# Kernel tuning notes

Hardware: AMD Instinct MI355X
Metric: run time of the kernel (lower is better)

## Reference

```python
import math
import jax, jax.numpy as jnp
import numpy as np

B, M, N = 32, 64, 5000   # batch, multi_width (POMO rollouts), n_nodes
L, H, D, E = 100, 8, 16, 128  # local_size, head_num, qkv_dim, emb_dim


def setup_inputs() -> dict:
    key = jax.random.key(0)
    ks = jax.random.split(key, 10)
    return {
        "dist": jax.random.uniform(ks[0], (B, M, N), jnp.float32),
        "theta": jax.random.uniform(ks[1], (B, M, N), jnp.float32, minval=-math.pi, maxval=math.pi),
        "ninf_mask": jnp.zeros((B, M, N), jnp.float32),
        "W_init": jax.random.normal(ks[2], (E, 2), jnp.float32) * 0.1,
        "b_init": jax.random.normal(ks[3], (E,), jnp.float32) * 0.1,
        "cur_token": jax.random.uniform(ks[4], (E,), jnp.float32, minval=-1.0, maxval=1.0),
        "Wq": jax.random.normal(ks[5], (H * D, E), jnp.float32) * 0.05,
        "Wk": jax.random.normal(ks[6], (H * D, E), jnp.float32) * 0.05,
        "Wv": jax.random.normal(ks[7], (H * D, E), jnp.float32) * 0.05,
        "Wc": jax.random.normal(ks[8], (E, H * D), jnp.float32) * 0.05,
        "bc": jax.random.normal(ks[9], (E,), jnp.float32) * 0.05,
    }


def _positional_signal():
    # transformer sinusoidal encoding over the L gathered neighbors (E even -> no pad)
    num_ts = E // 2
    log_inc = math.log(10000.0) / max(num_ts - 1, 1)
    inv_ts = jnp.exp(jnp.arange(num_ts, dtype=jnp.float32) * -log_inc)
    pos = jnp.arange(L, dtype=jnp.float32)
    scaled = pos[:, None] * inv_ts[None, :]            # [L, E/2]
    return jnp.concatenate([jnp.sin(scaled), jnp.cos(scaled)], axis=1)  # [L, E]


def reference(dist, theta, ninf_mask, W_init, b_init, cur_token, Wq, Wk, Wv, Wc, bc):
    # mask out infeasible nodes (dist - (-inf) = +inf pushes them out of top-k)
    d = dist - ninf_mask                               # [B, M, N]
    neg_vals, idx = jax.lax.top_k(-d, L)               # smallest-L distances
    sorted_dist = -neg_vals                            # [B, M, L] ascending
    sorted_mask = jnp.take_along_axis(ninf_mask, idx, axis=-1)
    norm = sorted_dist.max(axis=-1, keepdims=True) + 1e-6
    sorted_dist = sorted_dist / norm
    sorted_theta = jnp.take_along_axis(theta, idx, axis=-1)
    sdt = jnp.stack([sorted_dist, sorted_theta], axis=-1)   # [B, M, L, 2]

    init_k = sdt @ W_init.T + b_init + _positional_signal()  # [B, M, L, E]

    # current-token query is a single shared learned vector -> q is [H, D]
    q = (Wq @ cur_token).reshape(H, D)
    kh = (init_k @ Wk.T).reshape(B, M, L, H, D)
    vh = (init_k @ Wv.T).reshape(B, M, L, H, D)

    score = jnp.einsum('hd,bmlhd->bhml', q, kh) / jnp.sqrt(jnp.float32(D))
    score = score + sorted_mask[:, None, :, :]              # rank3 ninf mask
    w = jax.nn.softmax(score, axis=-1)                      # [B, H, M, L]
    att = jnp.einsum('bhml,bmlhd->bmhd', w, vh).reshape(B, M, H * D)
    mh = att @ Wc.T + bc                                    # [B, M, E]

    score2 = jnp.einsum('bme,bmle->bml', mh, init_k) / jnp.sqrt(jnp.float32(E))

    # scatter local scores back into full [B, M, N]
    bi = jnp.arange(B)[:, None, None]
    mi = jnp.arange(M)[None, :, None]
    out = jnp.zeros((B, M, N), jnp.float32).at[bi, mi, idx].set(score2)
    return out
```

## Files before the change

kernel.cpp:

```cpp
#include <hip/hip_runtime.h>
#include <math.h>

#define B_ 32
#define M_ 64
#define N_ 5000
#define L_ 100
#define H_ 8
#define D_ 16
#define E_ 128
#define NBIN 1024
#define NI4 1250
#define NT 128

#define OFF_POSQ  0
#define OFF_C0    800
#define OFF_C1    808
#define OFF_C2    816
#define OFF_PV0   824
#define OFF_PV1   952
#define OFF_PVB   1080
#define OFF_WC0   1208
#define OFF_WC1   1336
#define OFF_WCB   1464
#define OFF_SB    1592
#define OFF_PCB   1596
#define OFF_PV    1696
#define OFF_PCT   14496

__device__ __forceinline__ int vbin(float v) {
  if (!(v >= 0.f)) return 0;
  if (v >= 1.0f) return NBIN - 1;
  return (int)(v * (float)NBIN);
}
__device__ __forceinline__ unsigned int umap(float v) {
  unsigned int b = __float_as_uint(v);
  return (b & 0x80000000u) ? ~b : (b | 0x80000000u);
}
__device__ __forceinline__ float unmap(unsigned int u) {
  unsigned int b = (u & 0x80000000u) ? (u ^ 0x80000000u) : ~u;
  return __uint_as_float(b);
}
#define HMAP8(b) ((((b) & 7) << 7) | ((b) >> 3))
#define HMAP2(b) ((((b) & 1) << 7) | ((b) >> 1))

__global__ __launch_bounds__(128) void precomp(
    const float* __restrict__ Wq, const float* __restrict__ Wk,
    const float* __restrict__ cur, const float* __restrict__ Wi,
    const float* __restrict__ bi, const float* __restrict__ Wv,
    const float* __restrict__ Wc, const float* __restrict__ bc,
    float* __restrict__ ws)
{
  const int tid = threadIdx.x;
  const int blk = blockIdx.x;
  __shared__ float pr[E_];
  __shared__ float red[8];
  const int lane = tid & 63, wvv = tid >> 6;

  if (blk == 0) {
    float qsv = 0.f;
    for (int e = 0; e < E_; ++e) qsv = fmaf(Wq[tid * E_ + e], cur[e], qsv);
    float wk0=0,wk1=0,wkb=0,pv0=0,pv1=0,pvb=0,wc0=0,wc1=0,wcb=0;
    for (int e = 0; e < E_; ++e) {
      float wi0 = Wi[2*e], wi1 = Wi[2*e+1], bie = bi[e];
      float wk = Wk[tid*E_+e], wvx = Wv[tid*E_+e], wcc = Wc[e*(H_*D_)+tid];
      wk0=fmaf(wk,wi0,wk0);  wk1=fmaf(wk,wi1,wk1);  wkb=fmaf(wk,bie,wkb);
      pv0=fmaf(wvx,wi0,pv0); pv1=fmaf(wvx,wi1,pv1); pvb=fmaf(wvx,bie,pvb);
      wc0=fmaf(wcc,wi0,wc0); wc1=fmaf(wcc,wi1,wc1); wcb=fmaf(wcc,bie,wcb);
    }
    ws[OFF_PV0+tid]=pv0; ws[OFF_PV1+tid]=pv1; ws[OFF_PVB+tid]=pvb;
    ws[OFF_WC0+tid]=wc0; ws[OFF_WC1+tid]=wc1; ws[OFF_WCB+tid]=wcb;
    float c0 = qsv*wk0, c1 = qsv*wk1, c2 = qsv*wkb;
    for (int off = 1; off < 16; off <<= 1) {
      c0 += __shfl_xor(c0, off, 16); c1 += __shfl_xor(c1, off, 16); c2 += __shfl_xor(c2, off, 16);
    }
    if ((tid & 15) == 0) {
      int h = tid >> 4;
      ws[OFF_C0+h] = c0*0.25f; ws[OFF_C1+h] = c1*0.25f; ws[OFF_C2+h] = c2*0.25f;
    }
    float p0 = Wi[2*tid]*bc[tid], p1 = Wi[2*tid+1]*bc[tid], p2 = bi[tid]*bc[tid];
    for (int off = 32; off > 0; off >>= 1) {
      p0 += __shfl_xor(p0, off, 64); p1 += __shfl_xor(p1, off, 64); p2 += __shfl_xor(p2, off, 64);
    }
    if (lane == 0) { red[wvv*3+0]=p0; red[wvv*3+1]=p1; red[wvv*3+2]=p2; }
    __syncthreads();
    if (tid == 0) {
      ws[OFF_SB+0]=red[0]+red[3]; ws[OFF_SB+1]=red[1]+red[4]; ws[OFF_SB+2]=red[2]+red[5];
    }
  } else {
    const int l = blk - 1;
    const float log_inc = 0.14619588050755848f;
    {
      int j = tid & 63;
      float scaled = (float)l * expf(-(float)j * log_inc);
      pr[tid] = (tid < 64) ? sinf(scaled) : cosf(scaled);
    }
    __syncthreads();
    float qsv=0.f, pwk=0.f, accv=0.f, accc=0.f;
    for (int e = 0; e < E_; ++e) qsv = fmaf(Wq[tid*E_+e], cur[e], qsv);
    for (int e = 0; e < E_; ++e) {
      float p = pr[e];
      pwk  = fmaf(Wk[tid*E_+e], p, pwk);
      accv = fmaf(Wv[tid*E_+e], p, accv);
      accc = fmaf(Wc[e*(H_*D_)+tid], p, accc);
    }
    ws[OFF_PV  + l*(H_*D_) + tid] = accv;
    ws[OFF_PCT + tid*L_ + l] = accc;
    float pq = qsv * pwk;
    for (int off = 1; off < 16; off <<= 1) pq += __shfl_xor(pq, off, 16);
    if ((tid & 15) == 0) ws[OFF_POSQ + (tid>>4)*L_ + l] = pq * 0.25f;
    float pb = pr[tid] * bc[tid];
    for (int off = 32; off > 0; off >>= 1) pb += __shfl_xor(pb, off, 64);
    if (lane == 0) red[wvv] = pb;
    __syncthreads();
    if (tid == 0) ws[OFF_PCB + l] = red[0] + red[1];
  }
}

__global__ __launch_bounds__(NT, 4) void local_att_kernel(
    const float* __restrict__ dist, const float* __restrict__ theta,
    const float* __restrict__ ninf, const float* __restrict__ ws,
    float* __restrict__ out)
{
  __shared__ unsigned int hist[NBIN];
  __shared__ unsigned long long sel[128];
  __shared__ float sdv[128];
  __shared__ unsigned int idxs[128];
  __shared__ float stv[L_], smv[L_];
  __shared__ float att[H_ * D_];
  __shared__ unsigned int bitmap[160];
  __shared__ unsigned int hidx[256];
  __shared__ float hval[256];
  __shared__ unsigned int wsum[2];
  __shared__ unsigned int s_bstar, s_cumB, s_binc, s_cnt, s_chosen, s_cumb2;

  const int tid = threadIdx.x;
  const int lane = tid & 63, wv = tid >> 6;
  const size_t base = (size_t)blockIdx.x * N_;
  const float4* d4 = (const float4*)(dist + base);
  const float4* n4 = (const float4*)(ninf + base);

  for (int j = tid; j < NBIN; j += NT) hist[j] = 0u;
  sel[tid] = ~0ull;
  if (tid == 0) s_cnt = 0u;
  __syncthreads();

  unsigned int u[40];
#pragma unroll
  for (int t = 0; t < 10; ++t) {
    int i4 = tid + NT * t;
    if (i4 < NI4) {
      float4 dv = d4[i4], nv = n4[i4];
#pragma unroll
      for (int c = 0; c < 4; ++c) {
        float v = (&dv.x)[c] - (&nv.x)[c];
        u[4 * t + c] = umap(v);
        atomicAdd(&hist[HMAP8(vbin(v))], 1u);
      }
    }
  }
  __syncthreads();

  {
    unsigned int s = 0;
#pragma unroll
    for (int k = 0; k < 8; ++k) s += hist[(k << 7) | tid];
    unsigned int v = s;
#pragma unroll
    for (int off = 1; off < 64; off <<= 1) {
      unsigned int x = __shfl_up(v, off, 64);
      if (lane >= off) v += x;
    }
    if (lane == 63) wsum[wv] = v;
    __syncthreads();
    if (wv == 1) v += wsum[0];
    unsigned int cumBefore = v - s;
    if (cumBefore < (unsigned)L_ && v >= (unsigned)L_) {
      unsigned int c = cumBefore;
#pragma unroll
      for (int k = 0; k < 8; ++k) {
        unsigned int h = hist[(k << 7) | tid];
        if (c + h >= (unsigned)L_) { s_bstar = tid * 8 + k; s_cumB = c; s_binc = h; break; }
        c += h;
      }
    }
    __syncthreads();
  }
  const int bstar = (int)s_bstar;
  const bool fb = (s_cumB + s_binc > 128u);

  if (!fb) {
#pragma unroll
    for (int t = 0; t < 10; ++t) {
      int i4 = tid + NT * t;
      if (i4 < NI4) {
#pragma unroll
        for (int c = 0; c < 4; ++c) {
          unsigned int uu = u[4 * t + c];
          if (vbin(unmap(uu)) <= bstar) {
            unsigned int p = atomicAdd(&s_cnt, 1u);
            if (p < 128u) sel[p] = ((unsigned long long)uu << 16) | (unsigned)(4 * i4 + c);
          }
        }
      }
    }
  } else {
    unsigned long long prefix = 0ull;
    unsigned int Krem = L_;
    for (int pass = 0; pass < 6; ++pass) {
      const int shift = 40 - 8 * pass;
      for (int j = tid; j < 256; j += NT) hist[j] = 0u;
      __syncthreads();
#pragma unroll
      for (int t = 0; t < 10; ++t) {
        int i4 = tid + NT * t;
        if (i4 < NI4) {
#pragma unroll
          for (int c = 0; c < 4; ++c) {
            unsigned long long key = ((unsigned long long)u[4 * t + c] << 16) | (unsigned)(4 * i4 + c);
            if ((key >> (shift + 8)) == prefix) {
              unsigned int b = (unsigned int)(key >> shift) & 0xFFu;
              atomicAdd(&hist[HMAP2(b)], 1u);
            }
          }
        }
      }
      __syncthreads();
      unsigned int s0 = hist[tid];
      unsigned int s1 = hist[128 + tid];
      unsigned int s = s0 + s1;
      unsigned int v = s;
#pragma unroll
      for (int off = 1; off < 64; off <<= 1) {
        unsigned int x = __shfl_up(v, off, 64);
        if (lane >= off) v += x;
      }
      if (lane == 63) wsum[wv] = v;
      __syncthreads();
      if (wv == 1) v += wsum[0];
      unsigned int cb = v - s;
      if (cb < Krem && v >= Krem) {
        if (cb + s0 >= Krem) { s_chosen = 2u * tid;     s_cumb2 = cb; }
        else                 { s_chosen = 2u * tid + 1; s_cumb2 = cb + s0; }
      }
      __syncthreads();
      prefix = (prefix << 8) | s_chosen;
      Krem -= s_cumb2;
      __syncthreads();
    }
    const unsigned long long kpiv = prefix;
#pragma unroll
    for (int t = 0; t < 10; ++t) {
      int i4 = tid + NT * t;
      if (i4 < NI4) {
#pragma unroll
        for (int c = 0; c < 4; ++c) {
          unsigned long long key = ((unsigned long long)u[4 * t + c] << 16) | (unsigned)(4 * i4 + c);
          if (key <= kpiv) {
            unsigned int p = atomicAdd(&s_cnt, 1u);
            if (p < 128u) sel[p] = key;
          }
        }
      }
    }
  }
  __syncthreads();

  {
    unsigned long long ka = sel[tid];
    int ra = 0;
#pragma unroll 8
    for (int j = 0; j < 128; ++j) ra += (sel[j] < ka) ? 1 : 0;
    if (ka != ~0ull) {
      unsigned int uu = (unsigned int)(ka >> 16);
      sdv[ra] = unmap(uu);
      idxs[ra] = (unsigned int)(ka & 0xFFFFull);
    }
  }
  __syncthreads();

  const float invn = 1.0f / (sdv[L_ - 1] + 1e-6f);
  if (tid < L_) {
    unsigned int ix = idxs[tid];
    stv[tid] = theta[base + ix];
    smv[tid] = ninf[base + ix];
  }
  __syncthreads();

  if (wv == 0) {
    const int hh = lane >> 3, jj = lane & 7;
    float w13[13];
    float a0, a1;
    {
      const float c0 = ws[OFF_C0 + hh], c1 = ws[OFF_C1 + hh], c2 = ws[OFF_C2 + hh];
      float mx = -INFINITY;
#pragma unroll
      for (int k = 0; k < 13; ++k) {
        int l = jj + 8 * k;
        float scv = -INFINITY;
        if (l < L_)
          scv = fmaf(sdv[l] * invn, c0, fmaf(stv[l], c1, c2 + ws[OFF_POSQ + hh * L_ + l] + smv[l]));
        w13[k] = scv;
        mx = fmaxf(mx, scv);
      }
#pragma unroll
      for (int off = 1; off <= 4; off <<= 1) mx = fmaxf(mx, __shfl_xor(mx, off, 64));
      float sum = 0.f;
#pragma unroll
      for (int k = 0; k < 13; ++k) { float e = expf(w13[k] - mx); w13[k] = e; sum += e; }
#pragma unroll
      for (int off = 1; off <= 4; off <<= 1) sum += __shfl_xor(sum, off, 64);
      const float inv = 1.0f / sum;
      a0 = 0.f; a1 = 0.f;
#pragma unroll
      for (int k = 0; k < 13; ++k) {
        int l = jj + 8 * k; int lc = (l < L_) ? l : 0;
        float wgt = w13[k] * inv; w13[k] = wgt;
        a0 = fmaf(wgt, sdv[lc] * invn, a0);
        a1 = fmaf(wgt, stv[lc], a1);
      }
#pragma unroll
      for (int off = 1; off <= 4; off <<= 1) { a0 += __shfl_xor(a0, off, 64); a1 += __shfl_xor(a1, off, 64); }
    }
    {
      float part[16];
#pragma unroll
      for (int t = 0; t < 16; ++t) part[t] = 0.f;
#pragma unroll
      for (int k = 0; k < 13; ++k) {
        int l = jj + 8 * k;
        if (l < L_) {
          const float* pv = ws + OFF_PV + l * (H_ * D_) + hh * 16;
          float wgt = w13[k];
#pragma unroll
          for (int t = 0; t < 16; ++t) part[t] = fmaf(wgt, pv[t], part[t]);
        }
      }
#pragma unroll
      for (int off = 1; off <= 4; off <<= 1) {
#pragma unroll
        for (int t = 0; t < 16; ++t) part[t] += __shfl_xor(part[t], off, 64);
      }
#pragma unroll
      for (int t = 0; t < 16; ++t) {
        int hd = hh * 16 + t;
        att[hd] = fmaf(a0, ws[OFF_PV0 + hd], fmaf(a1, ws[OFF_PV1 + hd], ws[OFF_PVB + hd])) + part[t];
      }
    }
  } else {
    for (int j = lane; j < 160; j += 64) bitmap[j] = 0u;
    for (int j = lane; j < 256; j += 64) hidx[j] = 0xFFFFFFFFu;
  }
  __syncthreads();

  float m0, m1, mb;
  {
    float x0 = att[lane], x1 = att[lane + 64];
    m0 = fmaf(x0, ws[OFF_WC0 + lane], x1 * ws[OFF_WC0 + lane + 64]);
    m1 = fmaf(x0, ws[OFF_WC1 + lane], x1 * ws[OFF_WC1 + lane + 64]);
    mb = fmaf(x0, ws[OFF_WCB + lane], x1 * ws[OFF_WCB + lane + 64]);
#pragma unroll
    for (int off = 1; off < 64; off <<= 1) {
      m0 += __shfl_xor(m0, off, 64);
      m1 += __shfl_xor(m1, off, 64);
      mb += __shfl_xor(mb, off, 64);
    }
    m0 += ws[OFF_SB + 0]; m1 += ws[OFF_SB + 1]; mb += ws[OFF_SB + 2];
  }

  if (tid < L_) {
    float acc = ws[OFF_PCB + tid];
#pragma unroll 8
    for (int hd = 0; hd < H_ * D_; ++hd) acc = fmaf(att[hd], ws[OFF_PCT + hd * L_ + tid], acc);
    const float SC = 0.08838834764831845f;
    float s2v = (fmaf(sdv[tid] * invn, m0, fmaf(stv[tid], m1, mb)) + acc) * SC;
    unsigned int idx = idxs[tid];
    unsigned int p = idx & 255u;
    while (atomicCAS(&hidx[p], 0xFFFFFFFFu, idx) != 0xFFFFFFFFu) p = (p + 1) & 255u;
    hval[p] = s2v;
    atomicOr(&bitmap[idx >> 5], 1u << (idx & 31));
  }
  __syncthreads();

  float4* o4 = (float4*)(out + base);
#pragma unroll
  for (int t = 0; t < 10; ++t) {
    int i4 = tid + NT * t;
    if (i4 < NI4) {
      unsigned int wbits = (bitmap[i4 >> 3] >> ((i4 & 7) * 4)) & 0xFu;
      float4 o = make_float4(0.f, 0.f, 0.f, 0.f);
      if (wbits) {
#pragma unroll
        for (int c = 0; c < 4; ++c) {
          if ((wbits >> c) & 1u) {
            unsigned int idx = (unsigned int)(4 * i4 + c);
            unsigned int p = idx & 255u;
            while (hidx[p] != idx) p = (p + 1) & 255u;
            (&o.x)[c] = hval[p];
          }
        }
      }
      o4[i4] = o;
    }
  }
}

extern "C" void kernel_launch(void* const* d_in, const int* in_sizes, int n_in,
                              void* d_out, int out_size, void* d_ws, size_t ws_size,
                              hipStream_t stream) {
  const float* dist = (const float*)d_in[0];
  const float* theta = (const float*)d_in[1];
  const float* ninf = (const float*)d_in[2];
  const float* Wi   = (const float*)d_in[3];
  const float* bi   = (const float*)d_in[4];
  const float* cur  = (const float*)d_in[5];
  const float* Wq   = (const float*)d_in[6];
  const float* Wk   = (const float*)d_in[7];
  const float* Wv   = (const float*)d_in[8];
  const float* Wc   = (const float*)d_in[9];
  const float* bcv  = (const float*)d_in[10];
  float* out = (float*)d_out;
  float* ws  = (float*)d_ws;

  precomp<<<dim3(L_ + 1), dim3(128), 0, stream>>>(Wq, Wk, cur, Wi, bi, Wv, Wc, bcv, ws);
  local_att_kernel<<<dim3(B_ * M_), dim3(NT), 0, stream>>>(dist, theta, ninf, ws, out);
}
```

Before: 72.08 us.

## Double block size to 256 threads and redistribute top-k and attention work

Raises the per-row block from 128 to 256 threads, halving per-thread register arrays and loop trip counts for the load, histogram and scatter phases. The radix-select pass now uses one bin per thread, which removes the two-bin split. The theta and mask gather is folded into the rank-sort step, and the bitmap and hash clears move to the idle waves, which drops one barrier. Softmax and attention now run across two waves with 16 lanes per head. The risks are lower occupancy per CU if register use does not fall, more waves per barrier, and half the threads sitting idle in the later phases.

```diff
diff --git a/kernel.cpp b/kernel.cpp
--- a/kernel.cpp
+++ b/kernel.cpp
@@ -10,7 +10,7 @@
 #define E_ 128
 #define NBIN 1024
 #define NI4 1250
-#define NT 128
+#define NT 256
 
 #define OFF_POSQ  0
 #define OFF_C0    800
@@ -40,8 +40,7 @@
   unsigned int b = (u & 0x80000000u) ? (u ^ 0x80000000u) : ~u;
   return __uint_as_float(b);
 }
-#define HMAP8(b) ((((b) & 7) << 7) | ((b) >> 3))
-#define HMAP2(b) ((((b) & 1) << 7) | ((b) >> 1))
+#define HMAPA(b) ((((b) & 3) << 8) | ((b) >> 2))
 
 __global__ __launch_bounds__(128) void precomp(
     const float* __restrict__ Wq, const float* __restrict__ Wk,
@@ -116,7 +115,7 @@
   }
 }
 
-__global__ __launch_bounds__(NT, 4) void local_att_kernel(
+__global__ __launch_bounds__(NT, 8) void local_att_kernel(
     const float* __restrict__ dist, const float* __restrict__ theta,
     const float* __restrict__ ninf, const float* __restrict__ ws,
     float* __restrict__ out)
@@ -125,12 +124,12 @@
   __shared__ unsigned long long sel[128];
   __shared__ float sdv[128];
   __shared__ unsigned int idxs[128];
-  __shared__ float stv[L_], smv[L_];
+  __shared__ float stv[128], smv[128];
   __shared__ float att[H_ * D_];
   __shared__ unsigned int bitmap[160];
   __shared__ unsigned int hidx[256];
   __shared__ float hval[256];
-  __shared__ unsigned int wsum[2];
+  __shared__ unsigned int wsum[4];
   __shared__ unsigned int s_bstar, s_cumB, s_binc, s_cnt, s_chosen, s_cumb2;
 
   const int tid = threadIdx.x;
@@ -140,13 +139,13 @@
   const float4* n4 = (const float4*)(ninf + base);
 
   for (int j = tid; j < NBIN; j += NT) hist[j] = 0u;
-  sel[tid] = ~0ull;
+  if (tid < 128) sel[tid] = ~0ull;
   if (tid == 0) s_cnt = 0u;
   __syncthreads();
 
-  unsigned int u[40];
-#pragma unroll
-  for (int t = 0; t < 10; ++t) {
+  unsigned int u[20];
+#pragma unroll
+  for (int t = 0; t < 5; ++t) {
     int i4 = tid + NT * t;
     if (i4 < NI4) {
       float4 dv = d4[i4], nv = n4[i4];
@@ -154,16 +153,16 @@
       for (int c = 0; c < 4; ++c) {
         float v = (&dv.x)[c] - (&nv.x)[c];
         u[4 * t + c] = umap(v);
-        atomicAdd(&hist[HMAP8(vbin(v))], 1u);
+        atomicAdd(&hist[HMAPA(vbin(v))], 1u);
       }
     }
   }
   __syncthreads();
 
   {
-    unsigned int s = 0;
-#pragma unroll
-    for (int k = 0; k < 8; ++k) s += hist[(k << 7) | tid];
+    unsigned int h4[4]; unsigned int s = 0;
+#pragma unroll
+    for (int k = 0; k < 4; ++k) { h4[k] = hist[(k << 8) | tid]; s += h4[k]; }
     unsigned int v = s;
 #pragma unroll
     for (int off = 1; off < 64; off <<= 1) {
@@ -172,14 +171,14 @@
     }
     if (lane == 63) wsum[wv] = v;
     __syncthreads();
-    if (wv == 1) v += wsum[0];
+    { unsigned int add = 0; for (int ww = 0; ww < wv; ++ww) add += wsum[ww]; v += add; }
     unsigned int cumBefore = v - s;
     if (cumBefore < (unsigned)L_ && v >= (unsigned)L_) {
       unsigned int c = cumBefore;
 #pragma unroll
-      for (int k = 0; k < 8; ++k) {
-        unsigned int h = hist[(k << 7) | tid];
-        if (c + h >= (unsigned)L_) { s_bstar = tid * 8 + k; s_cumB = c; s_binc = h; break; }
+      for (int k = 0; k < 4; ++k) {
+        unsigned int h = h4[k];
+        if (c + h >= (unsigned)L_) { s_bstar = tid * 4 + k; s_cumB = c; s_binc = h; break; }
         c += h;
       }
     }
@@ -190,7 +189,7 @@
 
   if (!fb) {
 #pragma unroll
-    for (int t = 0; t < 10; ++t) {
+    for (int t = 0; t < 5; ++t) {
       int i4 = tid + NT * t;
       if (i4 < NI4) {
 #pragma unroll
@@ -208,26 +207,22 @@
     unsigned int Krem = L_;
     for (int pass = 0; pass < 6; ++pass) {
       const int shift = 40 - 8 * pass;
-      for (int j = tid; j < 256; j += NT) hist[j] = 0u;
+      hist[tid] = 0u;
       __syncthreads();
 #pragma unroll
-      for (int t = 0; t < 10; ++t) {
+      for (int t = 0; t < 5; ++t) {
         int i4 = tid + NT * t;
         if (i4 < NI4) {
 #pragma unroll
           for (int c = 0; c < 4; ++c) {
             unsigned long long key = ((unsigned long long)u[4 * t + c] << 16) | (unsigned)(4 * i4 + c);
-            if ((key >> (shift + 8)) == prefix) {
-              unsigned int b = (unsigned int)(key >> shift) & 0xFFu;
-              atomicAdd(&hist[HMAP2(b)], 1u);
-            }
+            if ((key >> (shift + 8)) == prefix)
+              atomicAdd(&hist[(unsigned)(key >> shift) & 0xFFu], 1u);
           }
         }
       }
       __syncthreads();
-      unsigned int s0 = hist[tid];
-      unsigned int s1 = hist[128 + tid];
-      unsigned int s = s0 + s1;
+      unsigned int s = hist[tid];
       unsigned int v = s;
 #pragma unroll
       for (int off = 1; off < 64; off <<= 1) {
@@ -236,12 +231,9 @@
       }
       if (lane == 63) wsum[wv] = v;
       __syncthreads();
-      if (wv == 1) v += wsum[0];
+      { unsigned int add = 0; for (int ww = 0; ww < wv; ++ww) add += wsum[ww]; v += add; }
       unsigned int cb = v - s;
-      if (cb < Krem && v >= Krem) {
-        if (cb + s0 >= Krem) { s_chosen = 2u * tid;     s_cumb2 = cb; }
-        else                 { s_chosen = 2u * tid + 1; s_cumb2 = cb + s0; }
-      }
+      if (cb < Krem && v >= Krem) { s_chosen = (unsigned)tid; s_cumb2 = cb; }
       __syncthreads();
       prefix = (prefix << 8) | s_chosen;
       Krem -= s_cumb2;
@@ -249,7 +241,7 @@
     }
     const unsigned long long kpiv = prefix;
 #pragma unroll
-    for (int t = 0; t < 10; ++t) {
+    for (int t = 0; t < 5; ++t) {
       int i4 = tid + NT * t;
       if (i4 < NI4) {
 #pragma unroll
@@ -265,78 +257,80 @@
   }
   __syncthreads();
 
-  {
+  if (tid < 128) {
     unsigned long long ka = sel[tid];
+    const bool valid = (ka != ~0ull);
+    unsigned int ix = (unsigned int)(ka & 0xFFFFull);
+    float th = 0.f, nm = 0.f;
+    if (valid) { th = theta[base + ix]; nm = ninf[base + ix]; }
     int ra = 0;
 #pragma unroll 8
     for (int j = 0; j < 128; ++j) ra += (sel[j] < ka) ? 1 : 0;
-    if (ka != ~0ull) {
-      unsigned int uu = (unsigned int)(ka >> 16);
-      sdv[ra] = unmap(uu);
-      idxs[ra] = (unsigned int)(ka & 0xFFFFull);
-    }
+    if (valid) {
+      sdv[ra] = unmap((unsigned int)(ka >> 16));
+      idxs[ra] = ix;
+      stv[ra] = th;
+      smv[ra] = nm;
+    }
+  } else if (tid < 192) {
+    for (int j = tid - 128; j < 160; j += 64) bitmap[j] = 0u;
+  } else {
+    for (int j = tid - 192; j < 256; j += 64) hidx[j] = 0xFFFFFFFFu;
   }
   __syncthreads();
 
   const float invn = 1.0f / (sdv[L_ - 1] + 1e-6f);
-  if (tid < L_) {
-    unsigned int ix = idxs[tid];
-    stv[tid] = theta[base + ix];
-    smv[tid] = ninf[base + ix];
-  }
-  __syncthreads();
-
-  if (wv == 0) {
-    const int hh = lane >> 3, jj = lane & 7;
-    float w13[13];
+  if (tid < 128) {
+    const int hh = tid >> 4, jj = tid & 15;
+    float w7[7];
     float a0, a1;
     {
       const float c0 = ws[OFF_C0 + hh], c1 = ws[OFF_C1 + hh], c2 = ws[OFF_C2 + hh];
       float mx = -INFINITY;
 #pragma unroll
-      for (int k = 0; k < 13; ++k) {
-        int l = jj + 8 * k;
+      for (int k = 0; k < 7; ++k) {
+        int l = jj + 16 * k;
         float scv = -INFINITY;
         if (l < L_)
           scv = fmaf(sdv[l] * invn, c0, fmaf(stv[l], c1, c2 + ws[OFF_POSQ + hh * L_ + l] + smv[l]));
-        w13[k] = scv;
+        w7[k] = scv;
         mx = fmaxf(mx, scv);
       }
 #pragma unroll
-      for (int off = 1; off <= 4; off <<= 1) mx = fmaxf(mx, __shfl_xor(mx, off, 64));
+      for (int off = 1; off <= 8; off <<= 1) mx = fmaxf(mx, __shfl_xor(mx, off, 64));
       float sum = 0.f;
 #pragma unroll
-      for (int k = 0; k < 13; ++k) { float e = expf(w13[k] - mx); w13[k] = e; sum += e; }
-#pragma unroll
-      for (int off = 1; off <= 4; off <<= 1) sum += __shfl_xor(sum, off, 64);
+      for (int k = 0; k < 7; ++k) { float e = expf(w7[k] - mx); w7[k] = e; sum += e; }
+#pragma unroll
+      for (int off = 1; off <= 8; off <<= 1) sum += __shfl_xor(sum, off, 64);
       const float inv = 1.0f / sum;
       a0 = 0.f; a1 = 0.f;
 #pragma unroll
-      for (int k = 0; k < 13; ++k) {
-        int l = jj + 8 * k; int lc = (l < L_) ? l : 0;
-        float wgt = w13[k] * inv; w13[k] = wgt;
+      for (int k = 0; k < 7; ++k) {
+        int l = jj + 16 * k; int lc = (l < L_) ? l : 0;
+        float wgt = w7[k] * inv; w7[k] = wgt;
         a0 = fmaf(wgt, sdv[lc] * invn, a0);
         a1 = fmaf(wgt, stv[lc], a1);
       }
 #pragma unroll
-      for (int off = 1; off <= 4; off <<= 1) { a0 += __shfl_xor(a0, off, 64); a1 += __shfl_xor(a1, off, 64); }
+      for (int off = 1; off <= 8; off <<= 1) { a0 += __shfl_xor(a0, off, 64); a1 += __shfl_xor(a1, off, 64); }
     }
     {
       float part[16];
 #pragma unroll
       for (int t = 0; t < 16; ++t) part[t] = 0.f;
 #pragma unroll
-      for (int k = 0; k < 13; ++k) {
-        int l = jj + 8 * k;
+      for (int k = 0; k < 7; ++k) {
+        int l = jj + 16 * k;
         if (l < L_) {
           const float* pv = ws + OFF_PV + l * (H_ * D_) + hh * 16;
-          float wgt = w13[k];
+          float wgt = w7[k];
 #pragma unroll
           for (int t = 0; t < 16; ++t) part[t] = fmaf(wgt, pv[t], part[t]);
         }
       }
 #pragma unroll
-      for (int off = 1; off <= 4; off <<= 1) {
+      for (int off = 1; off <= 8; off <<= 1) {
 #pragma unroll
         for (int t = 0; t < 16; ++t) part[t] += __shfl_xor(part[t], off, 64);
       }
@@ -346,14 +340,11 @@
         att[hd] = fmaf(a0, ws[OFF_PV0 + hd], fmaf(a1, ws[OFF_PV1 + hd], ws[OFF_PVB + hd])) + part[t];
       }
     }
-  } else {
-    for (int j = lane; j < 160; j += 64) bitmap[j] = 0u;
-    for (int j = lane; j < 256; j += 64) hidx[j] = 0xFFFFFFFFu;
-  }
-  __syncthreads();
-
-  float m0, m1, mb;
-  {
+  }
+  __syncthreads();
+
+  float m0 = 0.f, m1 = 0.f, mb = 0.f;
+  if (tid < 128) {
     float x0 = att[lane], x1 = att[lane + 64];
     m0 = fmaf(x0, ws[OFF_WC0 + lane], x1 * ws[OFF_WC0 + lane + 64]);
     m1 = fmaf(x0, ws[OFF_WC1 + lane], x1 * ws[OFF_WC1 + lane + 64]);
@@ -383,7 +374,7 @@
 
   float4* o4 = (float4*)(out + base);
 #pragma unroll
-  for (int t = 0; t < 10; ++t) {
+  for (int t = 0; t < 5; ++t) {
     int i4 = tid + NT * t;
     if (i4 < NI4) {
       unsigned int wbits = (bitmap[i4 >> 3] >> ((i4 & 7) * 4)) & 0xFu;
```

Result: slower. 84.43 us (+17.1%).

## Spill per-element bins to LDS instead of holding 40 keys in registers

Applied to the files above, without the earlier changes.

Replaces the 40-register array of mapped keys with 16-bit histogram bin indices stored in shared memory, and re-reads dist/ninf from global memory for the few selected candidates and in the fallback radix passes. Loads are split into two batches of five float4s to cut register pressure. The theta/ninf gather is folded into the rank step, which removes one barrier. The goal is lower VGPR use and higher occupancy, paid for with about 10KB more LDS and extra global reloads.

```diff
diff --git a/kernel.cpp b/kernel.cpp
--- a/kernel.cpp
+++ b/kernel.cpp
@@ -41,7 +41,6 @@
   return __uint_as_float(b);
 }
 #define HMAP8(b) ((((b) & 7) << 7) | ((b) >> 3))
-#define HMAP2(b) ((((b) & 1) << 7) | ((b) >> 1))
 
 __global__ __launch_bounds__(128) void precomp(
     const float* __restrict__ Wq, const float* __restrict__ Wk,
@@ -122,14 +121,15 @@
     float* __restrict__ out)
 {
   __shared__ unsigned int hist[NBIN];
+  __shared__ union alignas(16) {
+    unsigned short bins[N_];
+    struct { unsigned int bitmap[160]; unsigned int hidx[256]; float hval[256]; } o;
+  } bu;
   __shared__ unsigned long long sel[128];
   __shared__ float sdv[128];
   __shared__ unsigned int idxs[128];
-  __shared__ float stv[L_], smv[L_];
+  __shared__ float stv[128], smv[128];
   __shared__ float att[H_ * D_];
-  __shared__ unsigned int bitmap[160];
-  __shared__ unsigned int hidx[256];
-  __shared__ float hval[256];
   __shared__ unsigned int wsum[2];
   __shared__ unsigned int s_bstar, s_cumB, s_binc, s_cnt, s_chosen, s_cumb2;
 
@@ -144,26 +144,38 @@
   if (tid == 0) s_cnt = 0u;
   __syncthreads();
 
-  unsigned int u[40];
-#pragma unroll
-  for (int t = 0; t < 10; ++t) {
-    int i4 = tid + NT * t;
-    if (i4 < NI4) {
-      float4 dv = d4[i4], nv = n4[i4];
-#pragma unroll
-      for (int c = 0; c < 4; ++c) {
-        float v = (&dv.x)[c] - (&nv.x)[c];
-        u[4 * t + c] = umap(v);
-        atomicAdd(&hist[HMAP8(vbin(v))], 1u);
+#pragma unroll
+  for (int ch = 0; ch < 2; ++ch) {
+    float4 dr[5], nr[5];
+#pragma unroll
+    for (int t = 0; t < 5; ++t) {
+      int i4 = tid + NT * (5 * ch + t);
+      if (i4 < NI4) { dr[t] = d4[i4]; nr[t] = n4[i4]; }
+    }
+#pragma unroll
+    for (int t = 0; t < 5; ++t) {
+      int i4 = tid + NT * (5 * ch + t);
+      if (i4 < NI4) {
+        unsigned int bn[4];
+#pragma unroll
+        for (int c = 0; c < 4; ++c) {
+          float v = (&dr[t].x)[c] - (&nr[t].x)[c];
+          bn[c] = (unsigned int)vbin(v);
+          atomicAdd(&hist[HMAP8(bn[c])], 1u);
+        }
+        uint2 pk;
+        pk.x = bn[0] | (bn[1] << 16);
+        pk.y = bn[2] | (bn[3] << 16);
+        *(uint2*)&bu.bins[4 * i4] = pk;
       }
     }
   }
   __syncthreads();
 
   {
-    unsigned int s = 0;
-#pragma unroll
-    for (int k = 0; k < 8; ++k) s += hist[(k << 7) | tid];
+    unsigned int h8[8]; unsigned int s = 0;
+#pragma unroll
+    for (int k = 0; k < 8; ++k) { h8[k] = hist[(k << 7) | tid]; s += h8[k]; }
     unsigned int v = s;
 #pragma unroll
     for (int off = 1; off < 64; off <<= 1) {
@@ -178,7 +190,7 @@
       unsigned int c = cumBefore;
 #pragma unroll
       for (int k = 0; k < 8; ++k) {
-        unsigned int h = hist[(k << 7) | tid];
+        unsigned int h = h8[k];
         if (c + h >= (unsigned)L_) { s_bstar = tid * 8 + k; s_cumB = c; s_binc = h; break; }
         c += h;
       }
@@ -193,12 +205,15 @@
     for (int t = 0; t < 10; ++t) {
       int i4 = tid + NT * t;
       if (i4 < NI4) {
+        uint2 pk = *(const uint2*)&bu.bins[4 * i4];
+        unsigned int b4[4] = {pk.x & 0xFFFFu, pk.x >> 16, pk.y & 0xFFFFu, pk.y >> 16};
 #pragma unroll
         for (int c = 0; c < 4; ++c) {
-          unsigned int uu = u[4 * t + c];
-          if (vbin(unmap(uu)) <= bstar) {
+          if ((int)b4[c] <= bstar) {
+            int i = 4 * i4 + c;
+            float v = dist[base + i] - ninf[base + i];
             unsigned int p = atomicAdd(&s_cnt, 1u);
-            if (p < 128u) sel[p] = ((unsigned long long)uu << 16) | (unsigned)(4 * i4 + c);
+            if (p < 128u) sel[p] = ((unsigned long long)umap(v) << 16) | (unsigned)i;
           }
         }
       }
@@ -210,23 +225,21 @@
       const int shift = 40 - 8 * pass;
       for (int j = tid; j < 256; j += NT) hist[j] = 0u;
       __syncthreads();
-#pragma unroll
       for (int t = 0; t < 10; ++t) {
         int i4 = tid + NT * t;
         if (i4 < NI4) {
+          float4 dv = d4[i4], nv = n4[i4];
 #pragma unroll
           for (int c = 0; c < 4; ++c) {
-            unsigned long long key = ((unsigned long long)u[4 * t + c] << 16) | (unsigned)(4 * i4 + c);
-            if ((key >> (shift + 8)) == prefix) {
-              unsigned int b = (unsigned int)(key >> shift) & 0xFFu;
-              atomicAdd(&hist[HMAP2(b)], 1u);
-            }
+            float v = (&dv.x)[c] - (&nv.x)[c];
+            unsigned long long key = ((unsigned long long)umap(v) << 16) | (unsigned)(4 * i4 + c);
+            if ((key >> (shift + 8)) == prefix)
+              atomicAdd(&hist[(unsigned)(key >> shift) & 0xFFu], 1u);
           }
         }
       }
       __syncthreads();
-      unsigned int s0 = hist[tid];
-      unsigned int s1 = hist[128 + tid];
+      unsigned int s0 = hist[2 * tid], s1 = hist[2 * tid + 1];
       unsigned int s = s0 + s1;
       unsigned int v = s;
 #pragma unroll
@@ -248,13 +261,14 @@
       __syncthreads();
     }
     const unsigned long long kpiv = prefix;
-#pragma unroll
     for (int t = 0; t < 10; ++t) {
       int i4 = tid + NT * t;
       if (i4 < NI4) {
+        float4 dv = d4[i4], nv = n4[i4];
 #pragma unroll
         for (int c = 0; c < 4; ++c) {
-          unsigned long long key = ((unsigned long long)u[4 * t + c] << 16) | (unsigned)(4 * i4 + c);
+          float v = (&dv.x)[c] - (&nv.x)[c];
+          unsigned long long key = ((unsigned long long)umap(v) << 16) | (unsigned)(4 * i4 + c);
           if (key <= kpiv) {
             unsigned int p = atomicAdd(&s_cnt, 1u);
             if (p < 128u) sel[p] = key;
@@ -267,25 +281,23 @@
 
   {
     unsigned long long ka = sel[tid];
+    const bool valid = (ka != ~0ull);
+    unsigned int ix = (unsigned int)(ka & 0xFFFFull);
+    float th = 0.f, nm = 0.f;
+    if (valid) { th = theta[base + ix]; nm = ninf[base + ix]; }
     int ra = 0;
 #pragma unroll 8
     for (int j = 0; j < 128; ++j) ra += (sel[j] < ka) ? 1 : 0;
-    if (ka != ~0ull) {
-      unsigned int uu = (unsigned int)(ka >> 16);
-      sdv[ra] = unmap(uu);
-      idxs[ra] = (unsigned int)(ka & 0xFFFFull);
+    if (valid) {
+      sdv[ra] = unmap((unsigned int)(ka >> 16));
+      idxs[ra] = ix;
+      stv[ra] = th;
+      smv[ra] = nm;
     }
   }
   __syncthreads();
 
   const float invn = 1.0f / (sdv[L_ - 1] + 1e-6f);
-  if (tid < L_) {
-    unsigned int ix = idxs[tid];
-    stv[tid] = theta[base + ix];
-    smv[tid] = ninf[base + ix];
-  }
-  __syncthreads();
-
   if (wv == 0) {
     const int hh = lane >> 3, jj = lane & 7;
     float w13[13];
@@ -347,8 +359,8 @@
       }
     }
   } else {
-    for (int j = lane; j < 160; j += 64) bitmap[j] = 0u;
-    for (int j = lane; j < 256; j += 64) hidx[j] = 0xFFFFFFFFu;
+    for (int j = lane; j < 160; j += 64) bu.o.bitmap[j] = 0u;
+    for (int j = lane; j < 256; j += 64) bu.o.hidx[j] = 0xFFFFFFFFu;
   }
   __syncthreads();
 
@@ -375,9 +387,9 @@
     float s2v = (fmaf(sdv[tid] * invn, m0, fmaf(stv[tid], m1, mb)) + acc) * SC;
     unsigned int idx = idxs[tid];
     unsigned int p = idx & 255u;
-    while (atomicCAS(&hidx[p], 0xFFFFFFFFu, idx) != 0xFFFFFFFFu) p = (p + 1) & 255u;
-    hval[p] = s2v;
-    atomicOr(&bitmap[idx >> 5], 1u << (idx & 31));
+    while (atomicCAS(&bu.o.hidx[p], 0xFFFFFFFFu, idx) != 0xFFFFFFFFu) p = (p + 1) & 255u;
+    bu.o.hval[p] = s2v;
+    atomicOr(&bu.o.bitmap[idx >> 5], 1u << (idx & 31));
   }
   __syncthreads();
 
@@ -386,7 +398,7 @@
   for (int t = 0; t < 10; ++t) {
     int i4 = tid + NT * t;
     if (i4 < NI4) {
-      unsigned int wbits = (bitmap[i4 >> 3] >> ((i4 & 7) * 4)) & 0xFu;
+      unsigned int wbits = (bu.o.bitmap[i4 >> 3] >> ((i4 & 7) * 4)) & 0xFu;
       float4 o = make_float4(0.f, 0.f, 0.f, 0.f);
       if (wbits) {
 #pragma unroll
@@ -394,8 +406,8 @@
           if ((wbits >> c) & 1u) {
             unsigned int idx = (unsigned int)(4 * i4 + c);
             unsigned int p = idx & 255u;
-            while (hidx[p] != idx) p = (p + 1) & 255u;
-            (&o.x)[c] = hval[p];
+            while (bu.o.hidx[p] != idx) p = (p + 1) & 255u;
+            (&o.x)[c] = bu.o.hval[p];
           }
         }
       }
```

Measured after the change: 73.15 us. Within noise of the previous version (+1.5%).
